# Optimization experiments

Hardware: AMD Instinct MI355X
Metric: run time of the kernel (lower is better)

## Reference

```python
import jax, jax.numpy as jnp
import numpy as np
import math
from jax import lax


def _conv1d(x, w, stride=1):
    """Cross-correlation (torch F.conv1d semantics), VALID. x:[B,L], w:[K] -> [B,Lout]."""
    out = lax.conv_general_dilated(
        x[:, None, :], w[None, None, :], window_strides=(stride,), padding='VALID',
        dimension_numbers=('NCH', 'OIH', 'NCH'))
    return out[:, 0, :]


def setup_inputs() -> dict:
    B, D, K, NS = 32768, 1024, 8, 10  # batch, dim, filter_length, num_sparse_params
    key = jax.random.key(0)
    k_x, k_lo, k_hi, k_sp = jax.random.split(key, 4)
    x = jax.random.normal(k_x, (B, D), dtype=jnp.float32)
    sqrt2 = math.sqrt(2.0)
    base_lo = jnp.array([1.0, 1.0], dtype=jnp.float32) / sqrt2
    base_hi = jnp.array([1.0, -1.0], dtype=jnp.float32) / sqrt2
    dec_lo = jnp.pad(base_lo, (0, K - 2)) + 0.01 * jax.random.normal(k_lo, (K,), jnp.float32)
    dec_hi = jnp.pad(base_hi, (0, K - 2)) + 0.01 * jax.random.normal(k_hi, (K,), jnp.float32)
    rec_lo = dec_lo  # cloned from dec at init
    rec_hi = dec_hi
    std = math.sqrt(2.0 / D)
    sparse_coeffs = std * jax.random.normal(k_sp, (NS,), jnp.float32)
    # distinct indices from randperm(dim), all < 2*coeff_len so all valid
    sparse_indices = jnp.asarray(np.random.default_rng(0).permutation(D)[:NS], dtype=jnp.int32)
    return {"x": x, "dec_lo": dec_lo, "dec_hi": dec_hi, "rec_lo": rec_lo,
            "rec_hi": rec_hi, "sparse_coeffs": sparse_coeffs,
            "sparse_indices": sparse_indices}


def reference(x, dec_lo, dec_hi, rec_lo, rec_hi, sparse_coeffs, sparse_indices):
    B, D = x.shape
    K = dec_lo.shape[0]
    p = K - 1  # reflect pad size = 7
    # ---- DWT: reflect pad, correlate with flipped dec filters, stride-2 downsample ----
    xp = jnp.pad(x, ((0, 0), (p, p)), mode='reflect')          # [B, D+14]
    lo = _conv1d(xp, dec_lo[::-1], stride=2)                   # [B, 516]
    hi = _conv1d(xp, dec_hi[::-1], stride=2)                   # [B, 516]
    Lc = lo.shape[1]
    # ---- sparse coefficient injection at fixed indices (distinct indices) ----
    flat = jnp.concatenate([lo, hi], axis=1)                   # [B, 2*Lc]
    flat = flat.at[:, sparse_indices].add(sparse_coeffs[None, :])
    lo2, hi2 = flat[:, :Lc], flat[:, Lc:2 * Lc]
    # ---- IDWT: zero-upsample, reflect pad, correlate with rec filters ----
    up_lo = jnp.zeros((B, 2 * Lc), x.dtype).at[:, ::2].set(lo2)
    up_hi = jnp.zeros((B, 2 * Lc), x.dtype).at[:, ::2].set(hi2)
    up_lo = jnp.pad(up_lo, ((0, 0), (p, p)), mode='reflect')
    up_hi = jnp.pad(up_hi, ((0, 0), (p, p)), mode='reflect')
    rec = _conv1d(up_lo, rec_lo) + _conv1d(up_hi, rec_hi)      # [B, 2*Lc + p] = [B, 1039]
    rec = rec[:, :D]                                           # crop to target length (1039 > 1024)
    return x + rec
```

## Files before the change

### kernel.cpp

```cpp
#include <hip/hip_runtime.h>

#define D_LEN 1024
#define K_LEN 8
#define PAD   7
#define LC    516
#define NS    10

__global__ __launch_bounds__(256) void wavecore_kernel(
    const float* __restrict__ x,
    const float* __restrict__ dec_lo, const float* __restrict__ dec_hi,
    const float* __restrict__ rec_lo, const float* __restrict__ rec_hi,
    const float* __restrict__ sp_c,   const int* __restrict__ sp_i,
    float* __restrict__ out)
{
    __shared__ float sx[D_LEN];
    __shared__ float slo[LC];
    __shared__ float shi[LC];

    const int tid = threadIdx.x;
    const int b   = blockIdx.x;
    const float* xrow = x + (size_t)b * D_LEN;

    float4 xv = ((const float4*)xrow)[tid];
    ((float4*)sx)[tid] = xv;

    float f_dlo[K_LEN], f_dhi[K_LEN], f_rlo[K_LEN], f_rhi[K_LEN];
#pragma unroll
    for (int k = 0; k < K_LEN; ++k) {
        f_dlo[k] = dec_lo[k];
        f_dhi[k] = dec_hi[k];
        f_rlo[k] = rec_lo[k];
        f_rhi[k] = rec_hi[k];
    }
    __syncthreads();

#pragma unroll
    for (int it = 0; it < 3; ++it) {
        int c = tid + it * 256;
        if (c < LC) {
            float accL = 0.f, accH = 0.f;
#pragma unroll
            for (int k = 0; k < K_LEN; ++k) {
                int m = 2 * c + k - PAD;
                m = (m < 0) ? -m : ((m > D_LEN - 1) ? 2 * (D_LEN - 1) - m : m);
                float v = sx[m];
                accL += v * f_dlo[PAD - k];
                accH += v * f_dhi[PAD - k];
            }
            slo[c] = accL;
            shi[c] = accH;
        }
    }
    __syncthreads();

    if (tid < NS) {
        int s = sp_i[tid];
        float vadd = sp_c[tid];
        if (s < LC) slo[s] += vadd;
        else        shi[s - LC] += vadd;
    }
    __syncthreads();

    const int t0 = tid * 4;
    float res[4];
#pragma unroll
    for (int j = 0; j < 4; ++j) {
        const int t  = t0 + j;
        const int k0 = ((j & 1) ^ 1);
        float acc = 0.f;
#pragma unroll
        for (int i = 0; i < 4; ++i) {
            const int k = k0 + 2 * i;
            int m = t + k - PAD;
            m = (m < 0) ? -m : m;
            const int c = m >> 1;
            acc += slo[c] * f_rlo[k] + shi[c] * f_rhi[k];
        }
        res[j] = acc;
    }

    float4 r;
    r.x = res[0] + xv.x;
    r.y = res[1] + xv.y;
    r.z = res[2] + xv.z;
    r.w = res[3] + xv.w;
    ((float4*)(out + (size_t)b * D_LEN))[tid] = r;
}

extern "C" void kernel_launch(void* const* d_in, const int* in_sizes, int n_in,
                              void* d_out, int out_size, void* d_ws, size_t ws_size,
                              hipStream_t stream) {
    const float* x      = (const float*)d_in[0];
    const float* dec_lo = (const float*)d_in[1];
    const float* dec_hi = (const float*)d_in[2];
    const float* rec_lo = (const float*)d_in[3];
    const float* rec_hi = (const float*)d_in[4];
    const float* sp_c   = (const float*)d_in[5];
    const int*   sp_i   = (const int*)d_in[6];
    float* out = (float*)d_out;

    const int Brows = in_sizes[0] / D_LEN;
    wavecore_kernel<<<Brows, 256, 0, stream>>>(x, dec_lo, dec_hi, rec_lo, rec_hi,
                                               sp_c, sp_i, out);
}
```

Baseline: 53.74 us.

## Interleave lo/hi coefficients, vectorize conv LDS reads, use nontemporal global access

Stores the DWT lo/hi coefficients interleaved as float2 and computes only the 512 used coefficients, two per thread. Each thread reads its input window and coefficient neighbours with float4 shared-memory loads instead of scattered scalar reflect-indexed loads. Global loads and stores use nontemporal builtins to avoid polluting the cache on this streaming kernel. This drops the coefficients beyond index 512, which is valid because the output is cropped, and sparse indices that land there are ignored. It also adds a special-case branch for the first two threads.

Result: slower. 56.31 us (+4.8%).

```diff
diff --git a/kernel.cpp b/kernel.cpp
--- a/kernel.cpp
+++ b/kernel.cpp
@@ -6,6 +6,8 @@
 #define LC    516
 #define NS    10
 
+typedef float floatx4 __attribute__((ext_vector_type(4)));
+
 __global__ __launch_bounds__(256) void wavecore_kernel(
     const float* __restrict__ x,
     const float* __restrict__ dec_lo, const float* __restrict__ dec_hi,
@@ -13,16 +15,14 @@
     const float* __restrict__ sp_c,   const int* __restrict__ sp_i,
     float* __restrict__ out)
 {
-    __shared__ float sx[D_LEN];
-    __shared__ float slo[LC];
-    __shared__ float shi[LC];
+    __shared__ __align__(16) float  sx[D_LEN];
+    __shared__ __align__(16) float2 st[512];
 
     const int tid = threadIdx.x;
-    const int b   = blockIdx.x;
-    const float* xrow = x + (size_t)b * D_LEN;
+    const size_t rowoff = (size_t)blockIdx.x * D_LEN;
 
-    float4 xv = ((const float4*)xrow)[tid];
-    ((float4*)sx)[tid] = xv;
+    floatx4 xv = __builtin_nontemporal_load(((const floatx4*)(x + rowoff)) + tid);
+    ((floatx4*)sx)[tid] = xv;
 
     float f_dlo[K_LEN], f_dhi[K_LEN], f_rlo[K_LEN], f_rhi[K_LEN];
 #pragma unroll
@@ -34,57 +34,99 @@
     }
     __syncthreads();
 
+    float lo0 = 0.f, hi0 = 0.f, lo1 = 0.f, hi1 = 0.f;
+    if (tid >= 2) {
+        const float4 wa = ((const float4*)sx)[tid - 2];
+        const float4 wb = ((const float4*)sx)[tid - 1];
+        const float w[12] = { wa.x, wa.y, wa.z, wa.w,
+                              wb.x, wb.y, wb.z, wb.w,
+                              xv.x, xv.y, xv.z, xv.w };
 #pragma unroll
-    for (int it = 0; it < 3; ++it) {
-        int c = tid + it * 256;
-        if (c < LC) {
-            float accL = 0.f, accH = 0.f;
+        for (int j = 0; j < K_LEN; ++j) {
+            const float v0 = w[8  - j];
+            const float v1 = w[10 - j];
+            lo0 = fmaf(v0, f_dlo[j], lo0);
+            hi0 = fmaf(v0, f_dhi[j], hi0);
+            lo1 = fmaf(v1, f_dlo[j], lo1);
+            hi1 = fmaf(v1, f_dhi[j], hi1);
+        }
+    } else {
 #pragma unroll
-            for (int k = 0; k < K_LEN; ++k) {
-                int m = 2 * c + k - PAD;
-                m = (m < 0) ? -m : ((m > D_LEN - 1) ? 2 * (D_LEN - 1) - m : m);
-                float v = sx[m];
-                accL += v * f_dlo[PAD - k];
-                accH += v * f_dhi[PAD - k];
+        for (int q = 0; q < 2; ++q) {
+            const int c = 2 * tid + q;
+            float aL = 0.f, aH = 0.f;
+#pragma unroll
+            for (int j = 0; j < K_LEN; ++j) {
+                int m = 2 * c - j;
+                m = (m < 0) ? -m : m;
+                const float v = sx[m];
+                aL = fmaf(v, f_dlo[j], aL);
+                aH = fmaf(v, f_dhi[j], aH);
             }
-            slo[c] = accL;
-            shi[c] = accH;
+            if (q == 0) { lo0 = aL; hi0 = aH; }
+            else        { lo1 = aL; hi1 = aH; }
         }
+    }
+    {
+        float4 pr;
+        pr.x = lo0; pr.y = hi0; pr.z = lo1; pr.w = hi1;
+        ((float4*)st)[tid] = pr;
     }
     __syncthreads();
 
     if (tid < NS) {
-        int s = sp_i[tid];
-        float vadd = sp_c[tid];
-        if (s < LC) slo[s] += vadd;
-        else        shi[s - LC] += vadd;
+        const int s = sp_i[tid];
+        const float v = sp_c[tid];
+        if (s < 512)            st[s].x       += v;
+        else if (s >= LC)       st[s - LC].y  += v;
     }
     __syncthreads();
 
-    const int t0 = tid * 4;
-    float res[4];
+    float res0, res1, res2, res3;
+    if (tid >= 2) {
+        const float4 qa = ((const float4*)st)[tid - 2];
+        const float4 qb = ((const float4*)st)[tid - 1];
+        const float4 qc = ((const float4*)st)[tid];
+        const float p0l = qa.z, p0h = qa.w;
+        const float p1l = qb.x, p1h = qb.y;
+        const float p2l = qb.z, p2h = qb.w;
+        const float p3l = qc.x, p3h = qc.y;
+        const float p4l = qc.z, p4h = qc.w;
+        res0 = p0l*f_rlo[1] + p0h*f_rhi[1] + p1l*f_rlo[3] + p1h*f_rhi[3]
+             + p2l*f_rlo[5] + p2h*f_rhi[5] + p3l*f_rlo[7] + p3h*f_rhi[7];
+        res1 = p0l*f_rlo[0] + p0h*f_rhi[0] + p1l*f_rlo[2] + p1h*f_rhi[2]
+             + p2l*f_rlo[4] + p2h*f_rhi[4] + p3l*f_rlo[6] + p3h*f_rhi[6];
+        res2 = p1l*f_rlo[1] + p1h*f_rhi[1] + p2l*f_rlo[3] + p2h*f_rhi[3]
+             + p3l*f_rlo[5] + p3h*f_rhi[5] + p4l*f_rlo[7] + p4h*f_rhi[7];
+        res3 = p1l*f_rlo[0] + p1h*f_rhi[0] + p2l*f_rlo[2] + p2h*f_rhi[2]
+             + p3l*f_rlo[4] + p3h*f_rhi[4] + p4l*f_rlo[6] + p4h*f_rhi[6];
+    } else {
+        float acc[4];
 #pragma unroll
-    for (int j = 0; j < 4; ++j) {
-        const int t  = t0 + j;
-        const int k0 = ((j & 1) ^ 1);
-        float acc = 0.f;
+        for (int j = 0; j < 4; ++j) {
+            const int t  = 4 * tid + j;
+            const int k0 = ((j & 1) ^ 1);
+            float a = 0.f;
 #pragma unroll
-        for (int i = 0; i < 4; ++i) {
-            const int k = k0 + 2 * i;
-            int m = t + k - PAD;
-            m = (m < 0) ? -m : m;
-            const int c = m >> 1;
-            acc += slo[c] * f_rlo[k] + shi[c] * f_rhi[k];
+            for (int i = 0; i < 4; ++i) {
+                const int k = k0 + 2 * i;
+                int m = t + k - PAD;
+                m = (m < 0) ? -m : m;
+                const float2 pv = st[m >> 1];
+                a = fmaf(pv.x, f_rlo[k], a);
+                a = fmaf(pv.y, f_rhi[k], a);
+            }
+            acc[j] = a;
         }
-        res[j] = acc;
+        res0 = acc[0]; res1 = acc[1]; res2 = acc[2]; res3 = acc[3];
     }
 
-    float4 r;
-    r.x = res[0] + xv.x;
-    r.y = res[1] + xv.y;
-    r.z = res[2] + xv.z;
-    r.w = res[3] + xv.w;
-    ((float4*)(out + (size_t)b * D_LEN))[tid] = r;
+    floatx4 r;
+    r.x = res0 + xv.x;
+    r.y = res1 + xv.y;
+    r.z = res2 + xv.z;
+    r.w = res3 + xv.w;
+    __builtin_nontemporal_store(r, ((floatx4*)(out + rowoff)) + tid);
 }
 
 extern "C" void kernel_launch(void* const* d_in, const int* in_sizes, int n_in,
```

## Map one wavefront per row and replace shared memory with register shuffles

Applied to the files above, without the earlier changes.

Each 64-lane wavefront now owns a whole row, with each lane holding 16 contiguous elements in registers. The DWT and IDWT halos come from cross-lane shuffles and reflect handling on lane 0, replacing the shared-memory staging and the three block barriers. Sparse injection is done in registers through per-lane predicated adds. This removes LDS traffic and synchronisation from what is mostly a bandwidth-bound kernel. In exchange it uses more registers, and it drops handling of the right-edge reflect and of sparse indices landing in the tail coefficients (512-515 and 1028+), relying on the crop and on the test indices.

Result: slower. 61.55 us (+14.5%).

```diff
diff --git a/kernel.cpp b/kernel.cpp
--- a/kernel.cpp
+++ b/kernel.cpp
@@ -1,10 +1,9 @@
 #include <hip/hip_runtime.h>
 
 #define D_LEN 1024
-#define K_LEN 8
-#define PAD   7
-#define LC    516
 #define NS    10
+
+typedef float floatx4 __attribute__((ext_vector_type(4)));
 
 __global__ __launch_bounds__(256) void wavecore_kernel(
     const float* __restrict__ x,
@@ -13,78 +12,120 @@
     const float* __restrict__ sp_c,   const int* __restrict__ sp_i,
     float* __restrict__ out)
 {
-    __shared__ float sx[D_LEN];
-    __shared__ float slo[LC];
-    __shared__ float shi[LC];
+    const int lane = threadIdx.x & 63;
+    const int row  = blockIdx.x * 4 + (threadIdx.x >> 6);
+    const size_t base = (size_t)row * D_LEN + (size_t)lane * 16;
 
-    const int tid = threadIdx.x;
-    const int b   = blockIdx.x;
-    const float* xrow = x + (size_t)b * D_LEN;
+    float f_dlo[8], f_dhi[8], f_rlo[8], f_rhi[8];
+#pragma unroll
+    for (int k = 0; k < 8; ++k) {
+        f_dlo[k] = dec_lo[k]; f_dhi[k] = dec_hi[k];
+        f_rlo[k] = rec_lo[k]; f_rhi[k] = rec_hi[k];
+    }
 
-    float4 xv = ((const float4*)xrow)[tid];
-    ((float4*)sx)[tid] = xv;
+    const floatx4* xv4 = (const floatx4*)(x + base);
+    const floatx4 x0 = xv4[0], x1 = xv4[1], x2 = xv4[2], x3 = xv4[3];
+    float xr[16];
+    xr[0]=x0.x;  xr[1]=x0.y;  xr[2]=x0.z;  xr[3]=x0.w;
+    xr[4]=x1.x;  xr[5]=x1.y;  xr[6]=x1.z;  xr[7]=x1.w;
+    xr[8]=x2.x;  xr[9]=x2.y;  xr[10]=x2.z; xr[11]=x2.w;
+    xr[12]=x3.x; xr[13]=x3.y; xr[14]=x3.z; xr[15]=x3.w;
 
-    float f_dlo[K_LEN], f_dhi[K_LEN], f_rlo[K_LEN], f_rhi[K_LEN];
+    const bool l0 = (lane == 0);
+
+    float w[23];
+    {
+        float h0 = __shfl_up(xr[9], 1);
+        float h1 = __shfl_up(xr[10], 1);
+        float h2 = __shfl_up(xr[11], 1);
+        float h3 = __shfl_up(xr[12], 1);
+        float h4 = __shfl_up(xr[13], 1);
+        float h5 = __shfl_up(xr[14], 1);
+        float h6 = __shfl_up(xr[15], 1);
+        w[0] = l0 ? xr[7] : h0;
+        w[1] = l0 ? xr[6] : h1;
+        w[2] = l0 ? xr[5] : h2;
+        w[3] = l0 ? xr[4] : h3;
+        w[4] = l0 ? xr[3] : h4;
+        w[5] = l0 ? xr[2] : h5;
+        w[6] = l0 ? xr[1] : h6;
+    }
 #pragma unroll
-    for (int k = 0; k < K_LEN; ++k) {
-        f_dlo[k] = dec_lo[k];
-        f_dhi[k] = dec_hi[k];
-        f_rlo[k] = rec_lo[k];
-        f_rhi[k] = rec_hi[k];
+    for (int n = 0; n < 16; ++n) w[7 + n] = xr[n];
+
+    float lo[8], hi[8];
+#pragma unroll
+    for (int q = 0; q < 8; ++q) {
+        float aL = 0.f, aH = 0.f;
+#pragma unroll
+        for (int j = 0; j < 8; ++j) {
+            const float v = w[7 + 2 * q - j];
+            aL = fmaf(v, f_dlo[j], aL);
+            aH = fmaf(v, f_dhi[j], aH);
+        }
+        lo[q] = aL; hi[q] = aH;
     }
-    __syncthreads();
 
+    for (int n = 0; n < NS; ++n) {
+        const int   s = sp_i[n];
+        const float v = sp_c[n];
+        const bool isLo = (s < 512);
+        const bool isHi = (s >= 516);
+        const int  c    = isLo ? s : (s - 516);
+        const int  q    = c & 7;
+        const bool mine = (lane == (c >> 3)) && (isLo || isHi);
+        const float vL = (mine && isLo) ? v : 0.f;
+        const float vH = (mine && isHi) ? v : 0.f;
 #pragma unroll
-    for (int it = 0; it < 3; ++it) {
-        int c = tid + it * 256;
-        if (c < LC) {
-            float accL = 0.f, accH = 0.f;
-#pragma unroll
-            for (int k = 0; k < K_LEN; ++k) {
-                int m = 2 * c + k - PAD;
-                m = (m < 0) ? -m : ((m > D_LEN - 1) ? 2 * (D_LEN - 1) - m : m);
-                float v = sx[m];
-                accL += v * f_dlo[PAD - k];
-                accH += v * f_dhi[PAD - k];
-            }
-            slo[c] = accL;
-            shi[c] = accH;
+        for (int qq = 0; qq < 8; ++qq) {
+            if (q == qq) { lo[qq] += vL; hi[qq] += vH; }
         }
     }
-    __syncthreads();
 
-    if (tid < NS) {
-        int s = sp_i[tid];
-        float vadd = sp_c[tid];
-        if (s < LC) slo[s] += vadd;
-        else        shi[s - LC] += vadd;
+    float Plo[11], Phi[11];
+    {
+        float a0 = __shfl_up(lo[5], 1);
+        float a1 = __shfl_up(lo[6], 1);
+        float a2 = __shfl_up(lo[7], 1);
+        float b0 = __shfl_up(hi[5], 1);
+        float b1 = __shfl_up(hi[6], 1);
+        float b2 = __shfl_up(hi[7], 1);
+        Plo[0] = l0 ? lo[3] : a0;
+        Plo[1] = l0 ? lo[2] : a1;
+        Plo[2] = l0 ? lo[1] : a2;
+        Phi[0] = l0 ? hi[3] : b0;
+        Phi[1] = l0 ? hi[2] : b1;
+        Phi[2] = l0 ? hi[1] : b2;
     }
-    __syncthreads();
+#pragma unroll
+    for (int n = 0; n < 8; ++n) { Plo[3 + n] = lo[n]; Phi[3 + n] = hi[n]; }
 
-    const int t0 = tid * 4;
-    float res[4];
+    float res[16];
 #pragma unroll
-    for (int j = 0; j < 4; ++j) {
-        const int t  = t0 + j;
-        const int k0 = ((j & 1) ^ 1);
-        float acc = 0.f;
+    for (int r = 0; r < 16; ++r) {
+        const int k0 = (r & 1) ? 0 : 1;
+        float a = 0.f;
 #pragma unroll
-        for (int i = 0; i < 4; ++i) {
-            const int k = k0 + 2 * i;
-            int m = t + k - PAD;
-            m = (m < 0) ? -m : m;
-            const int c = m >> 1;
-            acc += slo[c] * f_rlo[k] + shi[c] * f_rhi[k];
+        for (int u = 0; u < 4; ++u) {
+            const int k = k0 + 2 * u;
+            const int n = (r + k - 7) / 2 + 3;
+            a = fmaf(Plo[n], f_rlo[k], a);
+            a = fmaf(Phi[n], f_rhi[k], a);
         }
-        res[j] = acc;
+        res[r] = a;
     }
 
-    float4 r;
-    r.x = res[0] + xv.x;
-    r.y = res[1] + xv.y;
-    r.z = res[2] + xv.z;
-    r.w = res[3] + xv.w;
-    ((float4*)(out + (size_t)b * D_LEN))[tid] = r;
+    floatx4* ov4 = (floatx4*)(out + base);
+    floatx4 r0, r1, r2, r3;
+    r0.x = res[0]  + xr[0];  r0.y = res[1]  + xr[1];
+    r0.z = res[2]  + xr[2];  r0.w = res[3]  + xr[3];
+    r1.x = res[4]  + xr[4];  r1.y = res[5]  + xr[5];
+    r1.z = res[6]  + xr[6];  r1.w = res[7]  + xr[7];
+    r2.x = res[8]  + xr[8];  r2.y = res[9]  + xr[9];
+    r2.z = res[10] + xr[10]; r2.w = res[11] + xr[11];
+    r3.x = res[12] + xr[12]; r3.y = res[13] + xr[13];
+    r3.z = res[14] + xr[14]; r3.w = res[15] + xr[15];
+    ov4[0] = r0; ov4[1] = r1; ov4[2] = r2; ov4[3] = r3;
 }
 
 extern "C" void kernel_launch(void* const* d_in, const int* in_sizes, int n_in,
@@ -99,7 +140,8 @@
     const int*   sp_i   = (const int*)d_in[6];
     float* out = (float*)d_out;
 
-    const int Brows = in_sizes[0] / D_LEN;
-    wavecore_kernel<<<Brows, 256, 0, stream>>>(x, dec_lo, dec_hi, rec_lo, rec_hi,
-                                               sp_c, sp_i, out);
+    const int Brows  = in_sizes[0] / D_LEN;
+    const int blocks = Brows / 4;
+    wavecore_kernel<<<blocks, 256, 0, stream>>>(x, dec_lo, dec_hi, rec_lo, rec_hi,
+                                                sp_c, sp_i, out);
 }
```

## Compute DWT/IDWT per thread from global halo loads, drop shared memory and barriers

Applied to the files above, without the earlier changes.

Each thread now loads its own overlapping window of the input row from global memory (mostly cached by L1/L2), computes the five low/high coefficients it needs in registers, applies the sparse injections with a wave-level check, and reconstructs its four outputs directly. This removes the shared-memory staging and all three __syncthreads barriers. In exchange it recomputes overlapping coefficients, issues redundant global loads, and adds a special-cased path for the first four threads to handle reflect padding. The right-edge reflection is not handled, on the assumption that outputs beyond index 1023 are cropped.

After: 66.24 us. 23.2% more time.

```diff
diff --git a/kernel.cpp b/kernel.cpp
--- a/kernel.cpp
+++ b/kernel.cpp
@@ -1,10 +1,8 @@
 #include <hip/hip_runtime.h>
 
 #define D_LEN 1024
-#define K_LEN 8
-#define PAD   7
-#define LC    516
 #define NS    10
+#define LCC   516
 
 __global__ __launch_bounds__(256) void wavecore_kernel(
     const float* __restrict__ x,
@@ -13,78 +11,132 @@
     const float* __restrict__ sp_c,   const int* __restrict__ sp_i,
     float* __restrict__ out)
 {
-    __shared__ float sx[D_LEN];
-    __shared__ float slo[LC];
-    __shared__ float shi[LC];
+    const int tid = threadIdx.x;
+    const float* __restrict__ xr = x + (size_t)blockIdx.x * D_LEN;
 
-    const int tid = threadIdx.x;
-    const int b   = blockIdx.x;
-    const float* xrow = x + (size_t)b * D_LEN;
+    float fdl[8], fdh[8], frl[8], frh[8];
+#pragma unroll
+    for (int k = 0; k < 8; ++k) {
+        fdl[k] = dec_lo[k]; fdh[k] = dec_hi[k];
+        frl[k] = rec_lo[k]; frh[k] = rec_hi[k];
+    }
 
-    float4 xv = ((const float4*)xrow)[tid];
-    ((float4*)sx)[tid] = xv;
+    float res0 = 0.f, res1 = 0.f, res2 = 0.f, res3 = 0.f;
+    float xo0 = 0.f, xo1 = 0.f, xo2 = 0.f, xo3 = 0.f;
 
-    float f_dlo[K_LEN], f_dhi[K_LEN], f_rlo[K_LEN], f_rhi[K_LEN];
+    if (tid >= 4) {
+        const float  h  = xr[4 * tid - 13];
+        const float4 qa = ((const float4*)xr)[tid - 3];
+        const float4 qb = ((const float4*)xr)[tid - 2];
+        const float4 qc = ((const float4*)xr)[tid - 1];
+        const float4 qd = ((const float4*)xr)[tid];
+        xo0 = qd.x; xo1 = qd.y; xo2 = qd.z; xo3 = qd.w;
+        const float W[16] = { h,
+                              qa.x, qa.y, qa.z, qa.w,
+                              qb.x, qb.y, qb.z, qb.w,
+                              qc.x, qc.y, qc.z, qc.w,
+                              qd.x, qd.y, qd.z };
+        float Plo[5], Phi[5];
 #pragma unroll
-    for (int k = 0; k < K_LEN; ++k) {
-        f_dlo[k] = dec_lo[k];
-        f_dhi[k] = dec_hi[k];
-        f_rlo[k] = rec_lo[k];
-        f_rhi[k] = rec_hi[k];
-    }
-    __syncthreads();
-
+        for (int i = 0; i < 5; ++i) {
+            float aL = 0.f, aH = 0.f;
 #pragma unroll
-    for (int it = 0; it < 3; ++it) {
-        int c = tid + it * 256;
-        if (c < LC) {
-            float accL = 0.f, accH = 0.f;
+            for (int j = 0; j < 8; ++j) {
+                const float v = W[7 + 2 * i - j];
+                aL = fmaf(v, fdl[j], aL);
+                aH = fmaf(v, fdh[j], aH);
+            }
+            Plo[i] = aL; Phi[i] = aH;
+        }
 #pragma unroll
-            for (int k = 0; k < K_LEN; ++k) {
-                int m = 2 * c + k - PAD;
-                m = (m < 0) ? -m : ((m > D_LEN - 1) ? 2 * (D_LEN - 1) - m : m);
-                float v = sx[m];
-                accL += v * f_dlo[PAD - k];
-                accH += v * f_dhi[PAD - k];
+        for (int n = 0; n < NS; ++n) {
+            const int   s    = sp_i[n];
+            const float v    = sp_c[n];
+            const bool  isHi = (s >= LCC);
+            const int   c    = isHi ? (s - LCC) : s;
+            const bool  ok   = isHi || (s < 512);
+            const int   d    = c - (2 * tid - 3);
+            const bool  hit  = ok && (d >= 0) && (d < 5);
+            if (__any(hit)) {
+#pragma unroll
+                for (int i = 0; i < 5; ++i) {
+                    const float av = (hit && d == i) ? v : 0.f;
+                    if (isHi) Phi[i] += av; else Plo[i] += av;
+                }
             }
-            slo[c] = accL;
-            shi[c] = accH;
         }
-    }
-    __syncthreads();
-
-    if (tid < NS) {
-        int s = sp_i[tid];
-        float vadd = sp_c[tid];
-        if (s < LC) slo[s] += vadd;
-        else        shi[s - LC] += vadd;
-    }
-    __syncthreads();
-
-    const int t0 = tid * 4;
-    float res[4];
+        res0 = Plo[0]*frl[1]+Phi[0]*frh[1] + Plo[1]*frl[3]+Phi[1]*frh[3]
+             + Plo[2]*frl[5]+Phi[2]*frh[5] + Plo[3]*frl[7]+Phi[3]*frh[7];
+        res1 = Plo[0]*frl[0]+Phi[0]*frh[0] + Plo[1]*frl[2]+Phi[1]*frh[2]
+             + Plo[2]*frl[4]+Phi[2]*frh[4] + Plo[3]*frl[6]+Phi[3]*frh[6];
+        res2 = Plo[1]*frl[1]+Phi[1]*frh[1] + Plo[2]*frl[3]+Phi[2]*frh[3]
+             + Plo[3]*frl[5]+Phi[3]*frh[5] + Plo[4]*frl[7]+Phi[4]*frh[7];
+        res3 = Plo[1]*frl[0]+Phi[1]*frh[0] + Plo[2]*frl[2]+Phi[2]*frh[2]
+             + Plo[3]*frl[4]+Phi[3]*frh[4] + Plo[4]*frl[6]+Phi[4]*frh[6];
+    } else {
+        const float4 q0 = ((const float4*)xr)[0];
+        const float4 q1 = ((const float4*)xr)[1];
+        const float4 q2 = ((const float4*)xr)[2];
+        const float4 q3 = ((const float4*)xr)[3];
+        const float X[16] = { q0.x, q0.y, q0.z, q0.w,
+                              q1.x, q1.y, q1.z, q1.w,
+                              q2.x, q2.y, q2.z, q2.w,
+                              q3.x, q3.y, q3.z, q3.w };
+        float Plo8[8], Phi8[8];
 #pragma unroll
-    for (int j = 0; j < 4; ++j) {
-        const int t  = t0 + j;
-        const int k0 = ((j & 1) ^ 1);
-        float acc = 0.f;
+        for (int c = 0; c < 8; ++c) {
+            float aL = 0.f, aH = 0.f;
 #pragma unroll
-        for (int i = 0; i < 4; ++i) {
-            const int k = k0 + 2 * i;
-            int m = t + k - PAD;
-            m = (m < 0) ? -m : m;
-            const int c = m >> 1;
-            acc += slo[c] * f_rlo[k] + shi[c] * f_rhi[k];
+            for (int j = 0; j < 8; ++j) {
+                const int m  = 2 * c - j;
+                const int mi = (m < 0) ? -m : m;
+                const float v = X[mi];
+                aL = fmaf(v, fdl[j], aL);
+                aH = fmaf(v, fdh[j], aH);
+            }
+            Plo8[c] = aL; Phi8[c] = aH;
         }
-        res[j] = acc;
+#pragma unroll
+        for (int n = 0; n < NS; ++n) {
+            const int   s    = sp_i[n];
+            const float v    = sp_c[n];
+            const bool  isHi = (s >= LCC);
+            const int   c    = isHi ? (s - LCC) : s;
+            const bool  ok   = isHi || (s < 512);
+            if (ok && c < 8) {
+#pragma unroll
+                for (int cc = 0; cc < 8; ++cc)
+                    if (c == cc) { if (isHi) Phi8[cc] += v; else Plo8[cc] += v; }
+            }
+        }
+        float rtmp[4] = {0.f, 0.f, 0.f, 0.f};
+#pragma unroll
+        for (int T = 0; T < 4; ++T) {
+            if (tid == T) {
+#pragma unroll
+                for (int j = 0; j < 4; ++j) {
+                    const int t  = 4 * T + j;
+                    const int k0 = (t & 1) ? 0 : 1;
+                    float a = 0.f;
+#pragma unroll
+                    for (int u = 0; u < 4; ++u) {
+                        const int k = k0 + 2 * u;
+                        const int m = t + k - 7;
+                        const int c = ((m < 0) ? -m : m) >> 1;
+                        a = fmaf(Plo8[c], frl[k], a);
+                        a = fmaf(Phi8[c], frh[k], a);
+                    }
+                    rtmp[j] = a;
+                }
+                xo0 = X[4*T]; xo1 = X[4*T+1]; xo2 = X[4*T+2]; xo3 = X[4*T+3];
+            }
+        }
+        res0 = rtmp[0]; res1 = rtmp[1]; res2 = rtmp[2]; res3 = rtmp[3];
     }
 
     float4 r;
-    r.x = res[0] + xv.x;
-    r.y = res[1] + xv.y;
-    r.z = res[2] + xv.z;
-    r.w = res[3] + xv.w;
-    ((float4*)(out + (size_t)b * D_LEN))[tid] = r;
+    r.x = res0 + xo0; r.y = res1 + xo1; r.z = res2 + xo2; r.w = res3 + xo3;
+    ((float4*)(out + (size_t)blockIdx.x * D_LEN))[tid] = r;
 }
 
 extern "C" void kernel_launch(void* const* d_in, const int* in_sizes, int n_in,
```
